# Kernel optimization log

Hardware: AMD Instinct MI355X
Metric: run time of the kernel (lower is better)

## Reference

```python
import jax, jax.numpy as jnp
import numpy as np

B, L = 4, 2048
D_MODEL, D_STATE, D_CONV, N_BLOCKS = 128, 16, 8, 6
EXPAND = 2
D_INNER = EXPAND * D_MODEL          # 256
DT_RANK = (D_MODEL + 15) // 16      # 8
CONV_K = 7                          # pre_conv kernel


def setup_inputs() -> dict:
    key = jax.random.key(0)
    ks = jax.random.split(key, 10)
    f = lambda k, s: jax.random.normal(k, s, jnp.float32)
    sc = 0.02
    A_init = jnp.broadcast_to(
        jnp.log(jnp.arange(1, D_STATE + 1, dtype=jnp.float32)),
        (N_BLOCKS, D_INNER, D_STATE)) + 0.0
    return {
        "x": f(ks[0], (B, L, 1)),
        "pre_conv_w": f(ks[1], (D_MODEL, 1, CONV_K)) * sc,
        "pre_conv_b": jnp.zeros((D_MODEL,), jnp.float32),
        "ln_w": jnp.ones((N_BLOCKS, D_MODEL), jnp.float32),
        "ln_b": jnp.zeros((N_BLOCKS, D_MODEL), jnp.float32),
        "W_in": f(ks[2], (N_BLOCKS, 2 * D_INNER, D_MODEL)) * sc,
        "conv_w": f(ks[3], (N_BLOCKS, D_INNER, 1, D_CONV)) * sc,  # depthwise OIH
        "conv_b": jnp.zeros((N_BLOCKS, D_INNER), jnp.float32),
        "W_x": f(ks[4], (N_BLOCKS, DT_RANK + 2 * D_STATE, D_INNER)) * sc,
        "W_dt": f(ks[5], (N_BLOCKS, D_INNER, DT_RANK)) * sc,
        "b_dt": jnp.full((N_BLOCKS, D_INNER), -4.6, jnp.float32),  # softplus ~ 0.01
        "A_log": A_init,
        "D_skip": jnp.ones((N_BLOCKS, D_INNER), jnp.float32),
        "W_out": f(ks[6], (N_BLOCKS, D_MODEL, D_INNER)) * sc,
        "out_w": f(ks[7], (1, D_MODEL)) * sc,
        "out_b": jnp.zeros((1,), jnp.float32),
    }


def _layernorm(x, w, b, eps=1e-5):
    m = jnp.mean(x, axis=-1, keepdims=True)
    v = jnp.mean(jnp.square(x - m), axis=-1, keepdims=True)
    return (x - m) * jax.lax.rsqrt(v + eps) * w + b


def _mamba(x, W_in, cw, cb, W_x, W_dt, b_dt, A_log, D_skip, W_out):
    # x: (B, L, D_MODEL)
    xz = jnp.einsum('bld,ed->ble', x, W_in)            # (B,L,2E)
    xi, z = jnp.split(xz, 2, axis=-1)
    # depthwise causal conv over time
    xc = jax.lax.conv_general_dilated(
        xi.transpose(0, 2, 1), cw, window_strides=(1,),
        padding=[(D_CONV - 1, 0)],
        dimension_numbers=('NCH', 'OIH', 'NCH'),
        feature_group_count=D_INNER) + cb[None, :, None]
    xc = jax.nn.silu(xc).transpose(0, 2, 1)            # (B,L,E)
    dbl = jnp.einsum('ble,re->blr', xc, W_x)
    dt = dbl[..., :DT_RANK]
    Bm = dbl[..., DT_RANK:DT_RANK + D_STATE]           # (B,L,N)
    Cm = dbl[..., DT_RANK + D_STATE:]                  # (B,L,N)
    delta = jax.nn.softplus(jnp.einsum('blr,er->ble', dt, W_dt) + b_dt)
    A = -jnp.exp(A_log)                                # (E,N)

    def step(h, inp):
        d, b, c, u = inp                               # (B,E),(B,N),(B,N),(B,E)
        h = h * jnp.exp(d[..., None] * A) + (d * u)[..., None] * b[:, None, :]
        return h, jnp.einsum('ben,bn->be', h, c)

    h0 = jnp.zeros((x.shape[0], D_INNER, D_STATE), x.dtype)
    xs = (delta.transpose(1, 0, 2), Bm.transpose(1, 0, 2),
          Cm.transpose(1, 0, 2), xc.transpose(1, 0, 2))
    _, ys = jax.lax.scan(step, h0, xs)                 # ys: (L,B,E)
    y = ys.transpose(1, 0, 2) + D_skip * xc
    y = y * jax.nn.silu(z)
    return jnp.einsum('ble,de->bld', y, W_out)


def reference(x, pre_conv_w, pre_conv_b, ln_w, ln_b, W_in, conv_w, conv_b,
              W_x, W_dt, b_dt, A_log, D_skip, W_out, out_w, out_b):
    # pre_conv (1 -> d_model), SAME padding, then exact GELU
    h = jax.lax.conv_general_dilated(
        x.transpose(0, 2, 1), pre_conv_w, window_strides=(1,),
        padding=[(CONV_K // 2, CONV_K // 2)],
        dimension_numbers=('NCH', 'OIH', 'NCH')) + pre_conv_b[None, :, None]
    h = jax.nn.gelu(h, approximate=False).transpose(0, 2, 1)  # (B,L,D)

    def block(carry, p):
        lw, lb, Wi, cw, cb, Wx, Wdt, bdt, Alog, Dsk, Wo = p
        y = _mamba(_layernorm(carry, lw, lb), Wi, cw, cb, Wx, Wdt, bdt, Alog, Dsk, Wo)
        return carry + y, None                         # dropout is identity (eval)

    h, _ = jax.lax.scan(block, h, (ln_w, ln_b, W_in, conv_w, conv_b,
                                   W_x, W_dt, b_dt, A_log, D_skip, W_out))
    return (jnp.einsum('bld,od->blo', h, out_w) + out_b)[..., 0]  # (B,L)
```

## Files before the change

kernel.cpp:

```cpp
#include <hip/hip_runtime.h>
#include <hip/hip_bf16.h>
#include <hip/hip_cooperative_groups.h>
#include <math.h>

namespace cg = cooperative_groups;

#define BB 4
#define LL 2048
#define DM 128
#define DI 256
#define DS 16
#define DTR 8
#define NB 6
#define KPRE 7
#define KC 8
#define NC 128
#define CT 16
#define NCHUNK (BB*NC)
#define BL (BB*LL)
#define SU 4

typedef __attribute__((ext_vector_type(8))) short short8v;
typedef __attribute__((ext_vector_type(4))) float f32x4;


__device__ __forceinline__ void dev_preconv(int idx,
    const float* __restrict__ x, const float* __restrict__ w, const float* __restrict__ bias,
    float* __restrict__ h, const float* __restrict__ Wi, const float* __restrict__ Wo,
    __hip_bfloat16* __restrict__ wi, __hip_bfloat16* __restrict__ wo) {
    int d = idx & (DM - 1);
    int l = (idx >> 7) & (LL - 1);
    int b = idx >> 18;
    float acc = bias[d];
#pragma unroll
    for (int k = 0; k < KPRE; ++k) {
        int pos = l + k - 3;
        float xv = (pos >= 0 && pos < LL) ? x[b * LL + pos] : 0.f;
        acc = fmaf(xv, w[d * KPRE + k], acc);
    }
    h[idx] = 0.5f * acc * (1.f + erff(acc * 0.70710678118654752f));
    if (idx < NB * 2 * DI * DM) wi[idx] = __float2bfloat16(Wi[idx]);
    if (idx < NB * DM * DI)     wo[idx] = __float2bfloat16(Wo[idx]);
}

__device__ __forceinline__ void dev_ln_gemm1(int v, int wave, int lane,
    const float* __restrict__ h, const float* __restrict__ lw, const float* __restrict__ lb,
    const __hip_bfloat16* __restrict__ W, float* __restrict__ xz,
    __hip_bfloat16* As) {
    int tileM = v >> 2, tileN = v & 3;
    int mBase = tileM * 64, nBase = tileN * 128;
    for (int it = 0; it < 16; ++it) {
        int row = wave * 16 + it;
        int t = mBase + row;
        float v0 = h[t * DM + lane];
        float v1 = h[t * DM + lane + 64];
        float s = v0 + v1;
#pragma unroll
        for (int off = 32; off; off >>= 1) s += __shfl_xor(s, off);
        float mean = s * (1.f / 128.f);
        float d0 = v0 - mean, d1 = v1 - mean;
        float q = d0 * d0 + d1 * d1;
#pragma unroll
        for (int off = 32; off; off >>= 1) q += __shfl_xor(q, off);
        float rstd = rsqrtf(q * (1.f / 128.f) + 1e-5f);
        int sw = (row & 7) << 3;
        As[row * 128 + (lane ^ sw)]        = __float2bfloat16(d0 * rstd * lw[lane] + lb[lane]);
        As[row * 128 + ((lane + 64) ^ sw)] = __float2bfloat16(d1 * rstd * lw[lane + 64] + lb[lane + 64]);
    }
    __syncthreads();
    int r  = lane & 15;
    int kh = lane >> 4;
    f32x4 acc[4][2] = {};
    for (int k0 = 0; k0 < DM; k0 += 32) {
        short8v af[4], bf[2];
#pragma unroll
        for (int i = 0; i < 4; ++i) {
            int row = i * 16 + r;
            int cbk = (k0 >> 3) + kh;
            af[i] = *(const short8v*)&As[row * 128 + ((cbk ^ (row & 7)) << 3)];
        }
#pragma unroll
        for (int j = 0; j < 2; ++j)
            bf[j] = *(const short8v*)&W[(size_t)(nBase + wave * 32 + j * 16 + r) * DM + k0 + kh * 8];
#pragma unroll
        for (int i = 0; i < 4; ++i)
#pragma unroll
            for (int j = 0; j < 2; ++j)
                acc[i][j] = __builtin_amdgcn_mfma_f32_16x16x32_bf16(af[i], bf[j], acc[i][j], 0, 0, 0);
    }
#pragma unroll
    for (int i = 0; i < 4; ++i)
#pragma unroll
        for (int j = 0; j < 2; ++j)
#pragma unroll
            for (int rg = 0; rg < 4; ++rg) {
                size_t off = (size_t)(mBase + i * 16 + kh * 4 + rg) * (2 * DI)
                           + nBase + wave * 32 + j * 16 + r;
                xz[off] = acc[i][j][rg];
            }
    __syncthreads();
}

__device__ __forceinline__ void dev_fusedA(int chunk, int tid,
    const float* __restrict__ xz, const float* __restrict__ cw, const float* __restrict__ cbs,
    const float* __restrict__ Wx, const float* __restrict__ Wdt, const float* __restrict__ bdt,
    const float* __restrict__ A_log, float* __restrict__ P, float* __restrict__ hend,
    float (*xc_s)[DI], float (*dl_s)[DI], float (*bc_s)[32]) {
    int c = chunk & (NC - 1);
    int b = chunk >> 7;
    int wave = tid >> 6, lane = tid & 63;
    float wts[4][8], cb4[4];
#pragma unroll
    for (int j = 0; j < 4; ++j) {
        int e = lane + 64 * j;
        float4 c0 = *(const float4*)&cw[e * KC];
        float4 c1 = *(const float4*)&cw[e * KC + 4];
        wts[j][0]=c0.x; wts[j][1]=c0.y; wts[j][2]=c0.z; wts[j][3]=c0.w;
        wts[j][4]=c1.x; wts[j][5]=c1.y; wts[j][6]=c1.z; wts[j][7]=c1.w;
        cb4[j] = cbs[e];
    }
    for (int i = 0; i < 4; ++i) {
        int lt = wave * 4 + i;
        int tl = c * CT + lt;
        float xv[4];
#pragma unroll
        for (int j = 0; j < 4; ++j) {
            int e = lane + 64 * j;
            float acc = cb4[j];
#pragma unroll
            for (int k = 0; k < KC; ++k) {
                int pos = tl + k - (KC - 1);
                float v = (pos >= 0) ? xz[((size_t)(b * LL + pos) << 9) + e] : 0.f;
                acc = fmaf(v, wts[j][k], acc);
            }
            xv[j] = acc / (1.f + __expf(-acc));
            xc_s[lt][e] = xv[j];
        }
        float dt8[8];
        float bcv = 0.f;
#pragma unroll
        for (int o = 0; o < 40; ++o) {
            const float* w = &Wx[o * DI];
            float s = xv[0] * w[lane];
            s = fmaf(xv[1], w[lane + 64], s);
            s = fmaf(xv[2], w[lane + 128], s);
            s = fmaf(xv[3], w[lane + 192], s);
#pragma unroll
            for (int off = 32; off; off >>= 1) s += __shfl_xor(s, off);
            if (o < 8) dt8[o] = s;
            else if (lane == o - 8) bcv = s;
        }
        if (lane < 32) bc_s[lt][lane] = bcv;
#pragma unroll
        for (int j = 0; j < 4; ++j) {
            int e = lane + 64 * j;
            float s = bdt[e];
#pragma unroll
            for (int r = 0; r < 8; ++r) s = fmaf(dt8[r], Wdt[e * 8 + r], s);
            dl_s[lt][e] = fmaxf(s, 0.f) + log1pf(__expf(-fabsf(s)));
        }
    }
    __syncthreads();
    int e = tid;
    float d16[CT], u16[CT];
#pragma unroll
    for (int l = 0; l < CT; ++l) { d16[l] = dl_s[l][e]; u16[l] = xc_s[l][e]; }
#pragma unroll
    for (int ng = 0; ng < 4; ++ng) {
        float4 al = *(const float4*)&A_log[e * DS + 4 * ng];
        float Aen[4] = {-__expf(al.x), -__expf(al.y), -__expf(al.z), -__expf(al.w)};
        float hh[4] = {}, Pl[4] = {1.f, 1.f, 1.f, 1.f};
#pragma unroll
        for (int l = 0; l < CT; ++l) {
            float du = d16[l] * u16[l];
            float4 bm = *(const float4*)&bc_s[l][4 * ng];
            float a0 = __expf(d16[l] * Aen[0]);
            float a1 = __expf(d16[l] * Aen[1]);
            float a2 = __expf(d16[l] * Aen[2]);
            float a3 = __expf(d16[l] * Aen[3]);
            hh[0] = fmaf(hh[0], a0, du * bm.x);
            hh[1] = fmaf(hh[1], a1, du * bm.y);
            hh[2] = fmaf(hh[2], a2, du * bm.z);
            hh[3] = fmaf(hh[3], a3, du * bm.w);
            Pl[0] *= a0; Pl[1] *= a1; Pl[2] *= a2; Pl[3] *= a3;
        }
        size_t oidx = (((size_t)(b * NC + c)) * DI + e) * DS + 4 * ng;
        *(float4*)&P[oidx]    = make_float4(Pl[0], Pl[1], Pl[2], Pl[3]);
        *(float4*)&hend[oidx] = make_float4(hh[0], hh[1], hh[2], hh[3]);
    }
}

__device__ __forceinline__ void dev_carry(int gtid,
    const float* __restrict__ P, const float* __restrict__ hend, float* __restrict__ hin) {
    int n = gtid & 15;
    int e = (gtid >> 4) & 255;
    int b = gtid >> 12;
    float carry = 0.f;
    for (int c = 0; c < NC; ++c) {
        size_t idx = (((size_t)(b * NC + c)) * DI + e) * DS + n;
        hin[idx] = carry;
        carry = fmaf(P[idx], carry, hend[idx]);
    }
}

__device__ __forceinline__ void dev_fusedB(int chunk, int tid,
    const float* __restrict__ A_log, const float* __restrict__ hin,
    const float* __restrict__ xz, const float* __restrict__ Dsk,
    const __hip_bfloat16* __restrict__ Wo, float* __restrict__ hout,
    const float (*xc_s)[DI], const float (*dl_s)[DI], const float (*bc_s)[32],
    __hip_bfloat16 (*y_s)[DI + 8]) {
    int c = chunk & (NC - 1);
    int b = chunk >> 7;
    int base = b * LL + c * CT;
    int e = tid;
    float d16[CT], u16[CT], yacc[CT];
    float dsk = Dsk[e];
#pragma unroll
    for (int l = 0; l < CT; ++l) {
        d16[l] = dl_s[l][e];
        u16[l] = xc_s[l][e];
        yacc[l] = dsk * u16[l];
    }
#pragma unroll
    for (int ng = 0; ng < 4; ++ng) {
        float4 al = *(const float4*)&A_log[e * DS + 4 * ng];
        float Aen[4] = {-__expf(al.x), -__expf(al.y), -__expf(al.z), -__expf(al.w)};
        float4 h4 = *(const float4*)&hin[(((size_t)(b * NC + c)) * DI + e) * DS + 4 * ng];
        float hh[4] = {h4.x, h4.y, h4.z, h4.w};
#pragma unroll
        for (int l = 0; l < CT; ++l) {
            float du = d16[l] * u16[l];
            float4 bm = *(const float4*)&bc_s[l][4 * ng];
            float4 cm = *(const float4*)&bc_s[l][16 + 4 * ng];
            float a0 = __expf(d16[l] * Aen[0]);
            float a1 = __expf(d16[l] * Aen[1]);
            float a2 = __expf(d16[l] * Aen[2]);
            float a3 = __expf(d16[l] * Aen[3]);
            hh[0] = fmaf(hh[0], a0, du * bm.x);
            hh[1] = fmaf(hh[1], a1, du * bm.y);
            hh[2] = fmaf(hh[2], a2, du * bm.z);
            hh[3] = fmaf(hh[3], a3, du * bm.w);
            float p = hh[0] * cm.x;
            p = fmaf(hh[1], cm.y, p);
            p = fmaf(hh[2], cm.z, p);
            p = fmaf(hh[3], cm.w, p);
            yacc[l] += p;
        }
    }
#pragma unroll
    for (int l = 0; l < CT; ++l) {
        float z = xz[((size_t)(base + l) << 9) + DI + e];
        float val = yacc[l] * (z / (1.f + __expf(-z)));
        y_s[l][e] = __float2bfloat16(val);
    }
    __syncthreads();
    int wave = tid >> 6, lane = tid & 63;
    int r  = lane & 15;
    int kh = lane >> 4;
    f32x4 acc[2] = {};
    for (int k0 = 0; k0 < DI; k0 += 32) {
        short8v af = *(const short8v*)&y_s[r][k0 + kh * 8];
        short8v bf[2];
#pragma unroll
        for (int j = 0; j < 2; ++j)
            bf[j] = *(const short8v*)&Wo[(size_t)(wave * 32 + j * 16 + r) * DI + k0 + kh * 8];
#pragma unroll
        for (int j = 0; j < 2; ++j)
            acc[j] = __builtin_amdgcn_mfma_f32_16x16x32_bf16(af, bf[j], acc[j], 0, 0, 0);
    }
#pragma unroll
    for (int j = 0; j < 2; ++j)
#pragma unroll
        for (int rg = 0; rg < 4; ++rg) {
            size_t off = (size_t)(base + kh * 4 + rg) * DM + wave * 32 + j * 16 + r;
            hout[off] += acc[j][rg];
        }
}

__device__ __forceinline__ void dev_out(int t, int lane,
    const float* __restrict__ h, const float* __restrict__ ow, const float* __restrict__ ob,
    float* __restrict__ out) {
    float s = h[t * DM + lane] * ow[lane] + h[t * DM + lane + 64] * ow[lane + 64];
#pragma unroll
    for (int off = 32; off; off >>= 1) s += __shfl_xor(s, off);
    if (lane == 0) out[t] = s + ob[0];
}


__device__ __forceinline__ void dev_conv_wx(int t, int lane,
    const float* __restrict__ xz, const float* __restrict__ cw, const float* __restrict__ cbs,
    const float* __restrict__ Wx, const float* __restrict__ Wdt, const float* __restrict__ bdt,
    float* __restrict__ xc, float* __restrict__ BC, float* __restrict__ delta) {
    int tl = t & (LL - 1);
    int b = t >> 11;
    float xv[4];
#pragma unroll
    for (int j = 0; j < 4; ++j) {
        int e = lane + 64 * j;
        float4 cw0 = *(const float4*)&cw[e * KC];
        float4 cw1 = *(const float4*)&cw[e * KC + 4];
        float wts[8] = {cw0.x, cw0.y, cw0.z, cw0.w, cw1.x, cw1.y, cw1.z, cw1.w};
        float acc = cbs[e];
#pragma unroll
        for (int k = 0; k < KC; ++k) {
            int pos = tl + k - (KC - 1);
            float v = (pos >= 0) ? xz[((size_t)(b * LL + pos) << 9) + e] : 0.f;
            acc = fmaf(v, wts[k], acc);
        }
        xv[j] = acc / (1.f + __expf(-acc));
        xc[((size_t)t << 8) + e] = xv[j];
    }
    float dt[8];
    float bcv = 0.f;
#pragma unroll
    for (int o = 0; o < 40; ++o) {
        const float* w = &Wx[o * DI];
        float s = xv[0] * w[lane];
        s = fmaf(xv[1], w[lane + 64], s);
        s = fmaf(xv[2], w[lane + 128], s);
        s = fmaf(xv[3], w[lane + 192], s);
#pragma unroll
        for (int off = 32; off; off >>= 1) s += __shfl_xor(s, off);
        if (o < 8) dt[o] = s;
        else if (lane == o - 8) bcv = s;
    }
    if (lane < 32) BC[((size_t)t << 5) + lane] = bcv;
#pragma unroll
    for (int j = 0; j < 4; ++j) {
        int e = lane + 64 * j;
        float s = bdt[e];
#pragma unroll
        for (int r = 0; r < 8; ++r) s = fmaf(dt[r], Wdt[e * 8 + r], s);
        delta[((size_t)t << 8) + e] = fmaxf(s, 0.f) + log1pf(__expf(-fabsf(s)));
    }
}

__device__ __forceinline__ void dev_scan1(int blk, int tid,
    const float* __restrict__ delta, const float* __restrict__ xc, const float* __restrict__ BC,
    const float* __restrict__ A_log, float* __restrict__ P, float* __restrict__ hend) {
    int eg = blk & 3;
    int c = (blk >> 2) & (NC - 1);
    int b = blk >> 9;
    int e = eg * 64 + (tid >> 2);
    int ng = tid & 3;
    float4 al = *(const float4*)&A_log[e * DS + 4 * ng];
    float Aen[4] = {-__expf(al.x), -__expf(al.y), -__expf(al.z), -__expf(al.w)};
    float h[4] = {}, Pl[4] = {1.f, 1.f, 1.f, 1.f};
    int base = b * LL + c * CT;
    const float* dp = delta + (size_t)base * DI + e;
    const float* up = xc + (size_t)base * DI + e;
    const float* bp = BC + (size_t)base * 32 + 4 * ng;
    for (int l0 = 0; l0 < CT; l0 += SU) {
        float d[SU], u[SU];
        float4 bm[SU];
#pragma unroll
        for (int j = 0; j < SU; ++j) {
            d[j]  = dp[(l0 + j) * DI];
            u[j]  = up[(l0 + j) * DI];
            bm[j] = *(const float4*)&bp[(l0 + j) * 32];
        }
#pragma unroll
        for (int j = 0; j < SU; ++j) {
            float du = d[j] * u[j];
            float a0 = __expf(d[j] * Aen[0]);
            float a1 = __expf(d[j] * Aen[1]);
            float a2 = __expf(d[j] * Aen[2]);
            float a3 = __expf(d[j] * Aen[3]);
            h[0] = fmaf(h[0], a0, du * bm[j].x);
            h[1] = fmaf(h[1], a1, du * bm[j].y);
            h[2] = fmaf(h[2], a2, du * bm[j].z);
            h[3] = fmaf(h[3], a3, du * bm[j].w);
            Pl[0] *= a0; Pl[1] *= a1; Pl[2] *= a2; Pl[3] *= a3;
        }
    }
    size_t oidx = (((size_t)(b * NC + c)) * DI + e) * DS + 4 * ng;
    *(float4*)&P[oidx]    = make_float4(Pl[0], Pl[1], Pl[2], Pl[3]);
    *(float4*)&hend[oidx] = make_float4(h[0], h[1], h[2], h[3]);
}

__device__ __forceinline__ void dev_scan3(int blk, int tid,
    const float* __restrict__ delta, const float* __restrict__ xc, const float* __restrict__ BC,
    const float* __restrict__ A_log, const float* __restrict__ hin, const float* __restrict__ xz,
    const float* __restrict__ Dsk, __hip_bfloat16* __restrict__ y) {
    int eg = blk & 3;
    int c = (blk >> 2) & (NC - 1);
    int b = blk >> 9;
    int e = eg * 64 + (tid >> 2);
    int ng = tid & 3;
    float4 al = *(const float4*)&A_log[e * DS + 4 * ng];
    float Aen[4] = {-__expf(al.x), -__expf(al.y), -__expf(al.z), -__expf(al.w)};
    float dsk = Dsk[e];
    float4 h4 = *(const float4*)&hin[(((size_t)(b * NC + c)) * DI + e) * DS + 4 * ng];
    float h[4] = {h4.x, h4.y, h4.z, h4.w};
    int base = b * LL + c * CT;
    const float* dp = delta + (size_t)base * DI + e;
    const float* up = xc + (size_t)base * DI + e;
    const float* bp = BC + (size_t)base * 32 + 4 * ng;
    const float* zp = xz + ((size_t)base << 9) + DI + e;
    __hip_bfloat16* yp = y + (size_t)base * DI + e;
    for (int l0 = 0; l0 < CT; l0 += SU) {
        float d[SU], u[SU], zv[SU];
        float4 bm[SU], cm[SU];
#pragma unroll
        for (int j = 0; j < SU; ++j) {
            d[j]  = dp[(l0 + j) * DI];
            u[j]  = up[(l0 + j) * DI];
            bm[j] = *(const float4*)&bp[(l0 + j) * 32];
            cm[j] = *(const float4*)&bp[(l0 + j) * 32 + 16];
            zv[j] = zp[(size_t)(l0 + j) << 9];
        }
#pragma unroll
        for (int j = 0; j < SU; ++j) {
            float du = d[j] * u[j];
            float a0 = __expf(d[j] * Aen[0]);
            float a1 = __expf(d[j] * Aen[1]);
            float a2 = __expf(d[j] * Aen[2]);
            float a3 = __expf(d[j] * Aen[3]);
            h[0] = fmaf(h[0], a0, du * bm[j].x);
            h[1] = fmaf(h[1], a1, du * bm[j].y);
            h[2] = fmaf(h[2], a2, du * bm[j].z);
            h[3] = fmaf(h[3], a3, du * bm[j].w);
            float yc = h[0] * cm[j].x;
            yc = fmaf(h[1], cm[j].y, yc);
            yc = fmaf(h[2], cm[j].z, yc);
            yc = fmaf(h[3], cm[j].w, yc);
            yc += __shfl_xor(yc, 1);
            yc += __shfl_xor(yc, 2);
            if (ng == 0) {
                float z = zv[j];
                float val = (yc + dsk * u[j]) * (z / (1.f + __expf(-z)));
                yp[(l0 + j) * DI] = __float2bfloat16(val);
            }
        }
    }
}

__device__ __forceinline__ void dev_gemm2(int v, int wave, int lane,
    const __hip_bfloat16* __restrict__ A, const __hip_bfloat16* __restrict__ W,
    float* __restrict__ C) {
    int mBase = v * 16;
    int r  = lane & 15;
    int kh = lane >> 4;
    f32x4 acc[2] = {};
    for (int k0 = 0; k0 < DI; k0 += 32) {
        short8v af = *(const short8v*)&A[(size_t)(mBase + r) * DI + k0 + kh * 8];
        short8v bf[2];
#pragma unroll
        for (int j = 0; j < 2; ++j)
            bf[j] = *(const short8v*)&W[(size_t)(wave * 32 + j * 16 + r) * DI + k0 + kh * 8];
#pragma unroll
        for (int j = 0; j < 2; ++j)
            acc[j] = __builtin_amdgcn_mfma_f32_16x16x32_bf16(af, bf[j], acc[j], 0, 0, 0);
    }
#pragma unroll
    for (int j = 0; j < 2; ++j)
#pragma unroll
        for (int rg = 0; rg < 4; ++rg) {
            size_t off = (size_t)(mBase + kh * 4 + rg) * DM + wave * 32 + j * 16 + r;
            C[off] += acc[j][rg];
        }
}


struct MegaArgs {
    const float *x, *pcw, *pcb, *ln_w, *ln_b, *W_in, *conv_w, *conv_b;
    const float *W_x, *W_dt, *b_dt, *A_log, *D_skip, *W_out, *out_w, *out_b;
    float *h, *xz, *xc, *BC, *delta, *P, *hend, *hin, *out;
    __hip_bfloat16 *y_bf, *wi_bf, *wo_bf;
};

__global__ __launch_bounds__(256) void k_mega(MegaArgs a) {
    __shared__ __hip_bfloat16 As[64 * 128];
    __shared__ float xc_s[CT][DI];
    __shared__ float dl_s[CT][DI];
    __shared__ float bc_s[CT][32];
    __shared__ __hip_bfloat16 y_s[CT][DI + 8];
    cg::grid_group g = cg::this_grid();
    int bid = blockIdx.x, tid = threadIdx.x;
    int nb = gridDim.x;
    int wave = tid >> 6, lane = tid & 63;

    for (int v = bid; v < (BB * LL * DM) / 256; v += nb)
        dev_preconv(v * 256 + tid, a.x, a.pcw, a.pcb, a.h, a.W_in, a.W_out, a.wi_bf, a.wo_bf);
    g.sync();

    for (int blk = 0; blk < NB; ++blk) {
        for (int v = bid; v < 512; v += nb)
            dev_ln_gemm1(v, wave, lane, a.h, a.ln_w + blk * DM, a.ln_b + blk * DM,
                         a.wi_bf + (size_t)blk * 2 * DI * DM, a.xz, As);
        g.sync();
        if (bid < NCHUNK)
            dev_fusedA(bid, tid, a.xz, a.conv_w + (size_t)blk * DI * KC,
                       a.conv_b + blk * DI, a.W_x + (size_t)blk * 40 * DI,
                       a.W_dt + (size_t)blk * DI * DTR, a.b_dt + blk * DI,
                       a.A_log + (size_t)blk * DI * DS, a.P, a.hend,
                       xc_s, dl_s, bc_s);
        g.sync();
        for (int v = bid; v < (BB * DI * DS) / 256; v += nb)
            dev_carry(v * 256 + tid, a.P, a.hend, a.hin);
        g.sync();
        if (bid < NCHUNK)
            dev_fusedB(bid, tid, a.A_log + (size_t)blk * DI * DS, a.hin, a.xz,
                       a.D_skip + blk * DI, a.wo_bf + (size_t)blk * DM * DI, a.h,
                       xc_s, dl_s, bc_s, y_s);
        g.sync();
    }

    for (int v = bid; v < BL / 4; v += nb)
        dev_out(v * 4 + wave, lane, a.h, a.out_w, a.out_b, a.out);
}


__global__ void w_preconv(const float* x, const float* w, const float* bias, float* h,
                          const float* Wi, const float* Wo,
                          __hip_bfloat16* wi, __hip_bfloat16* wo) {
    dev_preconv(blockIdx.x * 256 + threadIdx.x, x, w, bias, h, Wi, Wo, wi, wo);
}
__global__ __launch_bounds__(256) void w_ln_gemm1(const float* h, const float* lw, const float* lb,
                                                  const __hip_bfloat16* W, float* xz) {
    __shared__ __hip_bfloat16 As[64 * 128];
    dev_ln_gemm1(blockIdx.x, threadIdx.x >> 6, threadIdx.x & 63, h, lw, lb, W, xz, As);
}
__global__ __launch_bounds__(256) void w_conv_wx(const float* xz, const float* cw, const float* cbs,
                                                 const float* Wx, const float* Wdt, const float* bdt,
                                                 float* xc, float* BC, float* delta) {
    dev_conv_wx(blockIdx.x * 4 + (threadIdx.x >> 6), threadIdx.x & 63,
                xz, cw, cbs, Wx, Wdt, bdt, xc, BC, delta);
}
__global__ __launch_bounds__(256) void w_scan1(const float* delta, const float* xc, const float* BC,
                                               const float* A_log, float* P, float* hend) {
    dev_scan1(blockIdx.x, threadIdx.x, delta, xc, BC, A_log, P, hend);
}
__global__ void w_carry(const float* P, const float* hend, float* hin) {
    dev_carry(blockIdx.x * 256 + threadIdx.x, P, hend, hin);
}
__global__ __launch_bounds__(256) void w_scan3(const float* delta, const float* xc, const float* BC,
                                               const float* A_log, const float* hin, const float* xz,
                                               const float* Dsk, __hip_bfloat16* y) {
    dev_scan3(blockIdx.x, threadIdx.x, delta, xc, BC, A_log, hin, xz, Dsk, y);
}
__global__ __launch_bounds__(256) void w_gemm2(const __hip_bfloat16* A, const __hip_bfloat16* W,
                                               float* C) {
    dev_gemm2(blockIdx.x, threadIdx.x >> 6, threadIdx.x & 63, A, W, C);
}
__global__ void w_out(const float* h, const float* ow, const float* ob, float* out) {
    dev_out(blockIdx.x * 4 + (threadIdx.x >> 6), threadIdx.x & 63, h, ow, ob, out);
}

extern "C" void kernel_launch(void* const* d_in, const int* in_sizes, int n_in,
                              void* d_out, int out_size, void* d_ws, size_t ws_size,
                              hipStream_t stream) {
    (void)in_sizes; (void)n_in; (void)out_size; (void)ws_size;
    const float* x      = (const float*)d_in[0];
    const float* pcw    = (const float*)d_in[1];
    const float* pcb    = (const float*)d_in[2];
    const float* ln_w   = (const float*)d_in[3];
    const float* ln_b   = (const float*)d_in[4];
    const float* W_in   = (const float*)d_in[5];
    const float* conv_w = (const float*)d_in[6];
    const float* conv_b = (const float*)d_in[7];
    const float* W_x    = (const float*)d_in[8];
    const float* W_dt   = (const float*)d_in[9];
    const float* b_dt   = (const float*)d_in[10];
    const float* A_log  = (const float*)d_in[11];
    const float* D_skip = (const float*)d_in[12];
    const float* W_out  = (const float*)d_in[13];
    const float* out_w  = (const float*)d_in[14];
    const float* out_b  = (const float*)d_in[15];

    float* ws    = (float*)d_ws;
    float* h     = ws;
    float* xz    = h     + (size_t)BL * DM;
    float* xc    = xz    + (size_t)BL * 2 * DI;
    float* BC    = xc    + (size_t)BL * DI;
    float* delta = BC    + (size_t)BL * 2 * DS;
    float* P     = delta + (size_t)BL * DI;
    float* hend  = P     + (size_t)BB * NC * DI * DS;
    float* hin   = hend  + (size_t)BB * NC * DI * DS;
    __hip_bfloat16* y_bf  = (__hip_bfloat16*)(hin + (size_t)BB * NC * DI * DS);
    __hip_bfloat16* wi_bf = y_bf  + (size_t)BL * DI;
    __hip_bfloat16* wo_bf = wi_bf + (size_t)NB * 2 * DI * DM;

    int dev = 0;
    (void)hipGetDevice(&dev);
    int coopAttr = 0;
    (void)hipDeviceGetAttribute(&coopAttr, hipDeviceAttributeCooperativeLaunch, dev);
    int numCU = 0;
    (void)hipDeviceGetAttribute(&numCU, hipDeviceAttributeMultiprocessorCount, dev);
    int maxBpCU = 0;
    (void)hipOccupancyMaxActiveBlocksPerMultiprocessor(&maxBpCU, k_mega, 256, 0);
    int grid = maxBpCU * numCU;
    if (grid > NCHUNK) grid = NCHUNK;

    bool launched = false;
    if (coopAttr && grid == NCHUNK) {
        MegaArgs ma = {x, pcw, pcb, ln_w, ln_b, W_in, conv_w, conv_b,
                       W_x, W_dt, b_dt, A_log, D_skip, W_out, out_w, out_b,
                       h, xz, xc, BC, delta, P, hend, hin, (float*)d_out,
                       y_bf, wi_bf, wo_bf};
        void* kp[] = {&ma};
        hipError_t e = hipLaunchCooperativeKernel((void*)k_mega, dim3(grid), dim3(256), kp, 0, stream);
        launched = (e == hipSuccess);
        if (!launched) (void)hipGetLastError();
    }

    if (!launched) {
        w_preconv<<<(BB * LL * DM) / 256, 256, 0, stream>>>(x, pcw, pcb, h, W_in, W_out, wi_bf, wo_bf);
        for (int blk = 0; blk < NB; ++blk) {
            w_ln_gemm1<<<512, 256, 0, stream>>>(
                h, ln_w + blk * DM, ln_b + blk * DM, wi_bf + (size_t)blk * 2 * DI * DM, xz);
            w_conv_wx<<<BL / 4, 256, 0, stream>>>(
                xz, conv_w + (size_t)blk * DI * KC, conv_b + blk * DI,
                W_x + (size_t)blk * 40 * DI, W_dt + (size_t)blk * DI * DTR,
                b_dt + blk * DI, xc, BC, delta);
            w_scan1<<<BB * NC * 4, 256, 0, stream>>>(
                delta, xc, BC, A_log + (size_t)blk * DI * DS, P, hend);
            w_carry<<<(BB * DI * DS) / 256, 256, 0, stream>>>(P, hend, hin);
            w_scan3<<<BB * NC * 4, 256, 0, stream>>>(
                delta, xc, BC, A_log + (size_t)blk * DI * DS, hin, xz, D_skip + blk * DI, y_bf);
            w_gemm2<<<BL / 16, 256, 0, stream>>>(y_bf, wo_bf + (size_t)blk * DM * DI, h);
        }
        w_out<<<BL / 4, 256, 0, stream>>>(h, out_w, out_b, (float*)d_out);
    }
}
```

Before: 597.8 us.

## Cut registers and shared memory so the cooperative megakernel fits two blocks per CU

The kernel gets launch_bounds(256,2), the GEMM staging buffer and the y_s tile share one union in LDS, and several unroll pragmas are dropped while conv weights are reloaded inside the loop, all to lower register and LDS use and allow two resident blocks per CU. The sequential carry loop now loads eight chunks of P and hend before the dependent FMA chain so more memory loads are in flight. The `bid < NCHUNK` guards are removed, so the code assumes the grid is exactly NCHUNK blocks, and a barrier is added before hout is written so the aliased LDS stays safe. Risks are register spills under the tighter bound, less ILP from the removed unrolls, and wrong indexing if the grid size differs from NCHUNK.

```diff
diff --git a/kernel.cpp b/kernel.cpp
--- a/kernel.cpp
+++ b/kernel.cpp
@@ -109,29 +109,21 @@
     int c = chunk & (NC - 1);
     int b = chunk >> 7;
     int wave = tid >> 6, lane = tid & 63;
-    float wts[4][8], cb4[4];
-#pragma unroll
-    for (int j = 0; j < 4; ++j) {
-        int e = lane + 64 * j;
-        float4 c0 = *(const float4*)&cw[e * KC];
-        float4 c1 = *(const float4*)&cw[e * KC + 4];
-        wts[j][0]=c0.x; wts[j][1]=c0.y; wts[j][2]=c0.z; wts[j][3]=c0.w;
-        wts[j][4]=c1.x; wts[j][5]=c1.y; wts[j][6]=c1.z; wts[j][7]=c1.w;
-        cb4[j] = cbs[e];
-    }
     for (int i = 0; i < 4; ++i) {
         int lt = wave * 4 + i;
         int tl = c * CT + lt;
         float xv[4];
-#pragma unroll
         for (int j = 0; j < 4; ++j) {
             int e = lane + 64 * j;
-            float acc = cb4[j];
+            float4 c0 = *(const float4*)&cw[e * KC];
+            float4 c1 = *(const float4*)&cw[e * KC + 4];
+            float wts[8] = {c0.x, c0.y, c0.z, c0.w, c1.x, c1.y, c1.z, c1.w};
+            float acc = cbs[e];
 #pragma unroll
             for (int k = 0; k < KC; ++k) {
                 int pos = tl + k - (KC - 1);
                 float v = (pos >= 0) ? xz[((size_t)(b * LL + pos) << 9) + e] : 0.f;
-                acc = fmaf(v, wts[j][k], acc);
+                acc = fmaf(v, wts[k], acc);
             }
             xv[j] = acc / (1.f + __expf(-acc));
             xc_s[lt][e] = xv[j];
@@ -151,7 +143,6 @@
             else if (lane == o - 8) bcv = s;
         }
         if (lane < 32) bc_s[lt][lane] = bcv;
-#pragma unroll
         for (int j = 0; j < 4; ++j) {
             int e = lane + 64 * j;
             float s = bdt[e];
@@ -165,7 +156,6 @@
     float d16[CT], u16[CT];
 #pragma unroll
     for (int l = 0; l < CT; ++l) { d16[l] = dl_s[l][e]; u16[l] = xc_s[l][e]; }
-#pragma unroll
     for (int ng = 0; ng < 4; ++ng) {
         float4 al = *(const float4*)&A_log[e * DS + 4 * ng];
         float Aen[4] = {-__expf(al.x), -__expf(al.y), -__expf(al.z), -__expf(al.w)};
@@ -195,11 +185,22 @@
     int n = gtid & 15;
     int e = (gtid >> 4) & 255;
     int b = gtid >> 12;
+    const size_t cs = (size_t)DI * DS;
+    size_t idx0 = (((size_t)(b * NC)) * DI + e) * DS + n;
     float carry = 0.f;
-    for (int c = 0; c < NC; ++c) {
-        size_t idx = (((size_t)(b * NC + c)) * DI + e) * DS + n;
-        hin[idx] = carry;
-        carry = fmaf(P[idx], carry, hend[idx]);
+    for (int c0 = 0; c0 < NC; c0 += 8) {
+        float p[8], he[8];
+#pragma unroll
+        for (int j = 0; j < 8; ++j) {
+            size_t idx = idx0 + (size_t)(c0 + j) * cs;
+            p[j]  = P[idx];
+            he[j] = hend[idx];
+        }
+#pragma unroll
+        for (int j = 0; j < 8; ++j) {
+            hin[idx0 + (size_t)(c0 + j) * cs] = carry;
+            carry = fmaf(p[j], carry, he[j]);
+        }
     }
 }
 
@@ -221,7 +222,6 @@
         u16[l] = xc_s[l][e];
         yacc[l] = dsk * u16[l];
     }
-#pragma unroll
     for (int ng = 0; ng < 4; ++ng) {
         float4 al = *(const float4*)&A_log[e * DS + 4 * ng];
         float Aen[4] = {-__expf(al.x), -__expf(al.y), -__expf(al.z), -__expf(al.w)};
@@ -250,8 +250,7 @@
 #pragma unroll
     for (int l = 0; l < CT; ++l) {
         float z = xz[((size_t)(base + l) << 9) + DI + e];
-        float val = yacc[l] * (z / (1.f + __expf(-z)));
-        y_s[l][e] = __float2bfloat16(val);
+        y_s[l][e] = __float2bfloat16(yacc[l] * (z / (1.f + __expf(-z))));
     }
     __syncthreads();
     int wave = tid >> 6, lane = tid & 63;
@@ -268,6 +267,7 @@
         for (int j = 0; j < 2; ++j)
             acc[j] = __builtin_amdgcn_mfma_f32_16x16x32_bf16(af, bf[j], acc[j], 0, 0, 0);
     }
+    __syncthreads();
 #pragma unroll
     for (int j = 0; j < 2; ++j)
 #pragma unroll
@@ -469,12 +469,14 @@
     __hip_bfloat16 *y_bf, *wi_bf, *wo_bf;
 };
 
-__global__ __launch_bounds__(256) void k_mega(MegaArgs a) {
-    __shared__ __hip_bfloat16 As[64 * 128];
+__global__ __launch_bounds__(256, 2) void k_mega(MegaArgs a) {
+    __shared__ union {
+        __hip_bfloat16 As[64 * 128];
+        __hip_bfloat16 y_s[CT][DI + 8];
+    } u;
     __shared__ float xc_s[CT][DI];
     __shared__ float dl_s[CT][DI];
     __shared__ float bc_s[CT][32];
-    __shared__ __hip_bfloat16 y_s[CT][DI + 8];
     cg::grid_group g = cg::this_grid();
     int bid = blockIdx.x, tid = threadIdx.x;
     int nb = gridDim.x;
@@ -487,22 +489,20 @@
     for (int blk = 0; blk < NB; ++blk) {
         for (int v = bid; v < 512; v += nb)
             dev_ln_gemm1(v, wave, lane, a.h, a.ln_w + blk * DM, a.ln_b + blk * DM,
-                         a.wi_bf + (size_t)blk * 2 * DI * DM, a.xz, As);
+                         a.wi_bf + (size_t)blk * 2 * DI * DM, a.xz, u.As);
         g.sync();
-        if (bid < NCHUNK)
-            dev_fusedA(bid, tid, a.xz, a.conv_w + (size_t)blk * DI * KC,
-                       a.conv_b + blk * DI, a.W_x + (size_t)blk * 40 * DI,
-                       a.W_dt + (size_t)blk * DI * DTR, a.b_dt + blk * DI,
-                       a.A_log + (size_t)blk * DI * DS, a.P, a.hend,
-                       xc_s, dl_s, bc_s);
+        dev_fusedA(bid, tid, a.xz, a.conv_w + (size_t)blk * DI * KC,
+                   a.conv_b + blk * DI, a.W_x + (size_t)blk * 40 * DI,
+                   a.W_dt + (size_t)blk * DI * DTR, a.b_dt + blk * DI,
+                   a.A_log + (size_t)blk * DI * DS, a.P, a.hend,
+                   xc_s, dl_s, bc_s);
         g.sync();
         for (int v = bid; v < (BB * DI * DS) / 256; v += nb)
             dev_carry(v * 256 + tid, a.P, a.hend, a.hin);
         g.sync();
-        if (bid < NCHUNK)
-            dev_fusedB(bid, tid, a.A_log + (size_t)blk * DI * DS, a.hin, a.xz,
-                       a.D_skip + blk * DI, a.wo_bf + (size_t)blk * DM * DI, a.h,
-                       xc_s, dl_s, bc_s, y_s);
+        dev_fusedB(bid, tid, a.A_log + (size_t)blk * DI * DS, a.hin, a.xz,
+                   a.D_skip + blk * DI, a.wo_bf + (size_t)blk * DM * DI, a.h,
+                   xc_s, dl_s, bc_s, u.y_s);
         g.sync();
     }
 
```

Measured after the change: 579.4 us. 3.1% less time.
